# Kernel optimization log

Hardware: AMD Instinct MI355X
Metric: run time of the kernel (lower is better)

## Reference

```python
import jax, jax.numpy as jnp
import numpy as np
from jax import lax

# mamba-130m-style config
B, L = 2, 1024          # batch, seq_len
D = 768                 # hidden_size
E = 1536                # intermediate (expand=2)
N = 16                  # ssm state size
R = 48                  # time_step_rank = ceil(D/16)
K = 4                   # conv kernel
NL = 4                  # num layers
NC = 5                  # num classes
EPS = 1e-5


def setup_inputs() -> dict:
    key = jax.random.key(0)
    ks = jax.random.split(key, 10)
    s = 0.02
    return {
        "x": jax.random.normal(ks[0], (B, L, 12), dtype=jnp.float32),
        "proj_w": jax.random.normal(ks[1], (D, 12)) * s,
        "proj_b": jnp.zeros((D,), jnp.float32),
        "norm_w": jnp.ones((NL, D), jnp.float32),
        "in_w": jax.random.normal(ks[2], (NL, 2 * E, D)) * s,
        "conv_w": jax.random.normal(ks[3], (NL, E, K)) * s,
        "conv_b": jnp.zeros((NL, E), jnp.float32),
        "xproj_w": jax.random.normal(ks[4], (NL, R + 2 * N, E)) * s,
        "dt_w": jax.random.normal(ks[5], (NL, E, R)) * s,
        "dt_b": jnp.full((NL, E), -4.0, jnp.float32),  # softplus(-4) ~ small dt
        "A_log": jnp.tile(jnp.log(jnp.arange(1, N + 1, dtype=jnp.float32))[None, None, :], (NL, E, 1)),
        "D_param": jnp.ones((NL, E), jnp.float32),
        "out_w": jax.random.normal(ks[6], (NL, D, E)) * s,
        "fnorm_w": jnp.ones((D,), jnp.float32),
        "cls_w": jax.random.normal(ks[7], (NC, D)) * s,
        "cls_b": jnp.zeros((NC,), jnp.float32),
    }


def _rmsnorm(x, w):
    var = jnp.mean(x * x, axis=-1, keepdims=True)
    return x * lax.rsqrt(var + EPS) * w


def _causal_conv(u, w, b):
    # u: [B,L,E], w: [E,K] depthwise causal conv, left-pad K-1
    up = jnp.pad(u, ((0, 0), (K - 1, 0), (0, 0)))
    y = b
    for k in range(K):
        y = y + w[:, k] * up[:, k:k + L, :]
    return y


def _selective_scan(u, dt, A, Bm, Cm, Dp):
    # u, dt: [B,L,E]; Bm, Cm: [B,L,N]; A: [E,N]; Dp: [E]
    def step(h, inp):
        u_t, dt_t, B_t, C_t = inp  # [B,E],[B,E],[B,N],[B,N]
        dA = jnp.exp(dt_t[:, :, None] * A)                      # [B,E,N]
        h = h * dA + dt_t[:, :, None] * B_t[:, None, :] * u_t[:, :, None]
        y = jnp.einsum('ben,bn->be', h, C_t)
        return h, y

    h0 = jnp.zeros((u.shape[0], E, N), u.dtype)
    _, ys = lax.scan(step, h0,
                     (u.transpose(1, 0, 2), dt.transpose(1, 0, 2),
                      Bm.transpose(1, 0, 2), Cm.transpose(1, 0, 2)))
    return ys.transpose(1, 0, 2) + u * Dp


def reference(x, proj_w, proj_b, norm_w, in_w, conv_w, conv_b, xproj_w,
              dt_w, dt_b, A_log, D_param, out_w, fnorm_w, cls_w, cls_b):
    h = x @ proj_w.T + proj_b                                     # [B,L,D]
    for i in range(NL):
        res = h
        hn = _rmsnorm(h, norm_w[i])
        proj = hn @ in_w[i].T                                     # [B,L,2E]
        u, gate = proj[..., :E], proj[..., E:]
        u = jax.nn.silu(_causal_conv(u, conv_w[i], conv_b[i]))    # [B,L,E]
        xdbc = u @ xproj_w[i].T                                   # [B,L,R+2N]
        dt_r = xdbc[..., :R]
        Bm = xdbc[..., R:R + N]
        Cm = xdbc[..., R + N:]
        dt = jax.nn.softplus(dt_r @ dt_w[i].T + dt_b[i])          # [B,L,E]
        A = -jnp.exp(A_log[i])                                    # [E,N]
        y = _selective_scan(u, dt, A, Bm, Cm, D_param[i])
        y = y * jax.nn.silu(gate)
        h = res + y @ out_w[i].T
    h = _rmsnorm(h, fnorm_w)
    pooled = jnp.mean(h, axis=1)                                  # AdaptiveAvgPool1d(1)
    return pooled @ cls_w.T + cls_b                               # [B,NC]
```

## Files before the change

kernel.cpp:

```cpp
#include <hip/hip_runtime.h>

constexpr int B_  = 2;
constexpr int L_  = 1024;
constexpr int D_  = 768;
constexpr int E_  = 1536;
constexpr int N_  = 16;
constexpr int R_  = 48;
constexpr int NL_ = 4;
constexpr int NC_ = 5;
constexpr int M_  = B_ * L_;
constexpr int E2_ = 2 * E_;
constexpr int XD_ = R_ + 2 * N_;
constexpr float EPS_ = 1e-5f;

constexpr int NCH_ = 16;
constexpr int CL_  = L_ / NCH_;
constexpr int KS_  = 8;
constexpr int PC_  = 8;

typedef __attribute__((ext_vector_type(8))) short bf16x8;
typedef __attribute__((ext_vector_type(4))) float f32x4;
typedef const __attribute__((address_space(1))) void* gas_t;
typedef __attribute__((address_space(3))) void* las_t;

__device__ __forceinline__ float sigm(float x) { return 1.0f / (1.0f + __expf(-x)); }
__device__ __forceinline__ float softplusf(float x) { return x > 20.0f ? x : log1pf(__expf(x)); }
__device__ __forceinline__ ushort f2b(float f) {
  union { float f; unsigned u; } v; v.f = f;
  unsigned r = (v.u + 0x7fffu + ((v.u >> 16) & 1u)) >> 16;
  return (ushort)r;
}
__device__ __forceinline__ float b2f(ushort u) {
  union { unsigned u; float f; } v; v.u = ((unsigned)u) << 16;
  return v.f;
}
__device__ __forceinline__ float b2f_lo(unsigned p) {
  union { unsigned u; float f; } v; v.u = p << 16;
  return v.f;
}
__device__ __forceinline__ float b2f_hi(unsigned p) {
  union { unsigned u; float f; } v; v.u = p & 0xffff0000u;
  return v.f;
}

template <int CTRL>
__device__ __forceinline__ float dpp_add(float x) {
  int yi = __builtin_amdgcn_update_dpp(0, __builtin_bit_cast(int, x), CTRL, 0xf, 0xf, false);
  return x + __builtin_bit_cast(float, yi);
}
__device__ __forceinline__ float row_sum16(float x) {
  x = dpp_add<0x121>(x);
  x = dpp_add<0x122>(x);
  x = dpp_add<0x124>(x);
  x = dpp_add<0x128>(x);
  return x;
}

__device__ __forceinline__ float block_sum(float v, float* sm) {
  #pragma unroll
  for (int o = 32; o > 0; o >>= 1) v += __shfl_xor(v, o);
  if ((threadIdx.x & 63) == 0) sm[threadIdx.x >> 6] = v;
  __syncthreads();
  return sm[0] + sm[1] + sm[2] + sm[3];
}

constexpr int WS1_ = NL_ * E2_ * D_;
constexpr int WS2_ = NL_ * D_ * E_;
constexpr int WS3_ = NL_ * XD_ * E_;
constexpr int WS4_ = NL_ * E_ * 64;
constexpr int WTOT_ = WS1_ + WS2_ + WS3_ + WS4_;
constexpr int WB_ = WTOT_ / 4 / 256;
__global__ __launch_bounds__(256) void k_wprep(const float* __restrict__ in_w, const float* __restrict__ out_w,
                                               const float* __restrict__ xw, const float* __restrict__ dw,
                                               ushort* __restrict__ in_wb, ushort* __restrict__ out_wb,
                                               ushort* __restrict__ xwb, ushort* __restrict__ dtwb,
                                               const float* __restrict__ x, const float* __restrict__ pw,
                                               const float* __restrict__ pb, float* __restrict__ h) {
  if (blockIdx.x >= WB_) {
    __shared__ float xs[12];
    int bx = blockIdx.x - WB_;
    int m = bx / 3;
    int d = (bx % 3) * 256 + threadIdx.x;
    if (threadIdx.x < 12) xs[threadIdx.x] = x[m * 12 + threadIdx.x];
    __syncthreads();
    float acc = pb[d];
    #pragma unroll
    for (int j = 0; j < 12; j++) acc = fmaf(xs[j], pw[d * 12 + j], acc);
    h[(size_t)m * D_ + d] = acc;
    return;
  }
  int i = (blockIdx.x * 256 + threadIdx.x) * 4;
  if (i < WS1_) {
    float4 v = *(const float4*)(in_w + i);
    *(ushort4*)(in_wb + i) = make_ushort4(f2b(v.x), f2b(v.y), f2b(v.z), f2b(v.w));
  } else if (i < WS1_ + WS2_) {
    int j = i - WS1_;
    float4 v = *(const float4*)(out_w + j);
    *(ushort4*)(out_wb + j) = make_ushort4(f2b(v.x), f2b(v.y), f2b(v.z), f2b(v.w));
  } else if (i < WS1_ + WS2_ + WS3_) {
    int j = i - WS1_ - WS2_;
    float4 v = *(const float4*)(xw + j);
    *(ushort4*)(xwb + j) = make_ushort4(f2b(v.x), f2b(v.y), f2b(v.z), f2b(v.w));
  } else {
    int j = i - WS1_ - WS2_ - WS3_;
    int k = j & 63, e = j >> 6;
    ushort4 o;
    o.x = (k + 0 < R_) ? f2b(dw[e * R_ + k + 0]) : (ushort)0;
    o.y = (k + 1 < R_) ? f2b(dw[e * R_ + k + 1]) : (ushort)0;
    o.z = (k + 2 < R_) ? f2b(dw[e * R_ + k + 2]) : (ushort)0;
    o.w = (k + 3 < R_) ? f2b(dw[e * R_ + k + 3]) : (ushort)0;
    *(ushort4*)(dtwb + j) = o;
  }
}

__global__ __launch_bounds__(256) void k_rmsnorm_bf(const float* __restrict__ h, const float* __restrict__ w,
                                                    ushort* __restrict__ hn) {
  __shared__ float sm[4];
  int m = blockIdx.x, tid = threadIdx.x;
  const float* row = h + (size_t)m * D_;
  float v0 = row[tid], v1 = row[tid + 256], v2 = row[tid + 512];
  float s = block_sum(v0 * v0 + v1 * v1 + v2 * v2, sm);
  float sc = rsqrtf(s * (1.0f / D_) + EPS_);
  ushort* o = hn + (size_t)m * D_;
  o[tid]       = f2b(v0 * sc * w[tid]);
  o[tid + 256] = f2b(v1 * sc * w[tid + 256]);
  o[tid + 512] = f2b(v2 * sc * w[tid + 512]);
}

template <int BM, int BN, int MODE>
__global__ __launch_bounds__(256) void k_gemm_bf(const ushort* __restrict__ A, const ushort* __restrict__ Bw,
                                                 void* __restrict__ Cv, const float* __restrict__ res,
                                                 int Kd, int Nd) {
  constexpr int AM = BM / 32, BNF = BN / 32;
  __shared__ ushort sA[BM * 32];
  __shared__ ushort sB[BN * 32];
  const int tid = threadIdx.x;
  const int wave = tid >> 6, lane = tid & 63;
  const int q = lane >> 4, r = lane & 15;
  const int wm = wave >> 1, wn = wave & 1;
  const int m0 = blockIdx.y * BM, n0 = blockIdx.x * BN;
  f32x4 acc[AM][BNF] = {};

  for (int k0 = 0; k0 < Kd; k0 += 32) {
    #pragma unroll
    for (int j = 0; j < BM / 64; j++) {
      int i = j * 256 + tid;
      const ushort* gp = A + (size_t)(m0 + (i >> 2)) * Kd + k0 + ((i & 3) << 3);
      __builtin_amdgcn_global_load_lds((gas_t)gp, (las_t)(sA + ((j * 256 + wave * 64) << 3)), 16, 0, 0);
    }
    #pragma unroll
    for (int j = 0; j < BN / 64; j++) {
      int i = j * 256 + tid;
      const ushort* gp = Bw + (size_t)(n0 + (i >> 2)) * Kd + k0 + ((i & 3) << 3);
      __builtin_amdgcn_global_load_lds((gas_t)gp, (las_t)(sB + ((j * 256 + wave * 64) << 3)), 16, 0, 0);
    }
    __syncthreads();
    bf16x8 af[AM], bfv[BNF];
    #pragma unroll
    for (int mi = 0; mi < AM; mi++)
      af[mi] = *(const bf16x8*)&sA[(wm * (BM / 2) + mi * 16 + r) * 32 + q * 8];
    #pragma unroll
    for (int nj = 0; nj < BNF; nj++)
      bfv[nj] = *(const bf16x8*)&sB[(wn * (BN / 2) + nj * 16 + r) * 32 + q * 8];
    #pragma unroll
    for (int mi = 0; mi < AM; mi++)
      #pragma unroll
      for (int nj = 0; nj < BNF; nj++)
        acc[mi][nj] = __builtin_amdgcn_mfma_f32_16x16x32_bf16(af[mi], bfv[nj], acc[mi][nj], 0, 0, 0);
    __syncthreads();
  }
  #pragma unroll
  for (int mi = 0; mi < AM; mi++) {
    #pragma unroll
    for (int nj = 0; nj < BNF; nj++) {
      int col = n0 + wn * (BN / 2) + nj * 16 + r;
      #pragma unroll
      for (int rg = 0; rg < 4; rg++) {
        int row = m0 + wm * (BM / 2) + mi * 16 + q * 4 + rg;
        size_t off = (size_t)row * Nd + col;
        float v = acc[mi][nj][rg];
        if (MODE == 3) {
          ((ushort*)Cv)[off] = f2b(v);
        } else {
          if (MODE == 1) v += res[off];
          if (MODE == 2) v = softplusf(v + res[col]);
          ((float*)Cv)[off] = v;
        }
      }
    }
  }
}

__global__ __launch_bounds__(256) void k_gemm_x(const ushort* __restrict__ A, const ushort* __restrict__ Bw,
                                                float* __restrict__ part) {
  __shared__ ushort sA[64 * 32];
  __shared__ ushort sB[80 * 32];
  const int tid = threadIdx.x;
  const int wave = tid >> 6, lane = tid & 63;
  const int q = lane >> 4, r = lane & 15;
  const int m0 = blockIdx.x * 64;
  const int kbeg = blockIdx.y * (E_ / KS_), kend = kbeg + E_ / KS_;
  f32x4 acc[5] = {};

  for (int k0 = kbeg; k0 < kend; k0 += 32) {
    {
      const ushort* gp = A + (size_t)(m0 + wave * 16 + (lane >> 2)) * E_ + k0 + ((lane & 3) << 3);
      __builtin_amdgcn_global_load_lds((gas_t)gp, (las_t)(sA + (wave << 9)), 16, 0, 0);
    }
    #pragma unroll
    for (int j = wave; j < 5; j += 4) {
      const ushort* gp = Bw + (size_t)(j * 16 + (lane >> 2)) * E_ + k0 + ((lane & 3) << 3);
      __builtin_amdgcn_global_load_lds((gas_t)gp, (las_t)(sB + (j << 9)), 16, 0, 0);
    }
    __syncthreads();
    bf16x8 af = *(const bf16x8*)&sA[(wave * 16 + r) * 32 + q * 8];
    #pragma unroll
    for (int nj = 0; nj < 5; nj++) {
      bf16x8 bfv = *(const bf16x8*)&sB[(nj * 16 + r) * 32 + q * 8];
      acc[nj] = __builtin_amdgcn_mfma_f32_16x16x32_bf16(af, bfv, acc[nj], 0, 0, 0);
    }
    __syncthreads();
  }
  float* pp = part + (size_t)blockIdx.y * M_ * XD_;
  #pragma unroll
  for (int nj = 0; nj < 5; nj++) {
    int col = nj * 16 + r;
    #pragma unroll
    for (int rg = 0; rg < 4; rg++) {
      int row = m0 + wave * 16 + q * 4 + rg;
      pp[(size_t)row * XD_ + col] = acc[nj][rg];
    }
  }
}

__global__ __launch_bounds__(256) void k_xfin(const float* __restrict__ part, float* __restrict__ xdbc,
                                              ushort* __restrict__ xb) {
  int i = blockIdx.x * 256 + threadIdx.x;
  int m = i / XD_, col = i - m * XD_;
  float s = 0.0f;
  #pragma unroll
  for (int ks = 0; ks < KS_; ks++) s += part[(size_t)ks * M_ * XD_ + i];
  xdbc[i] = s;
  if (col < R_) xb[(size_t)m * 64 + col] = f2b(s);
  else if (col < 64) xb[(size_t)m * 64 + col] = 0;
}

__global__ __launch_bounds__(384) void k_conv2(const ushort* __restrict__ proj, const float* __restrict__ cw,
                                               const float* __restrict__ cb, ushort* __restrict__ ub16,
                                               ushort* __restrict__ gb16) {
  int m = blockIdx.x;
  int b = m >> 10, t = m & (L_ - 1);
  int e4 = threadIdx.x * 4;
  float wv[4][4];
  #pragma unroll
  for (int j = 0; j < 4; j++) {
    float4 w = *(const float4*)(cw + (e4 + j) * 4);
    wv[j][0] = w.x; wv[j][1] = w.y; wv[j][2] = w.z; wv[j][3] = w.w;
  }
  float4 bb = *(const float4*)(cb + e4);
  float acc[4] = {bb.x, bb.y, bb.z, bb.w};
  #pragma unroll
  for (int k = 0; k < 4; k++) {
    int tt = t + k - 3;
    if (tt >= 0) {
      uint2 p = *(const uint2*)(proj + (size_t)(b * L_ + tt) * E2_ + e4);
      acc[0] = fmaf(wv[0][k], b2f_lo(p.x), acc[0]);
      acc[1] = fmaf(wv[1][k], b2f_hi(p.x), acc[1]);
      acc[2] = fmaf(wv[2][k], b2f_lo(p.y), acc[2]);
      acc[3] = fmaf(wv[3][k], b2f_hi(p.y), acc[3]);
    }
  }
  uint2 uo;
  {
    float u0 = acc[0] * sigm(acc[0]), u1 = acc[1] * sigm(acc[1]);
    float u2 = acc[2] * sigm(acc[2]), u3 = acc[3] * sigm(acc[3]);
    uo.x = (unsigned)f2b(u0) | ((unsigned)f2b(u1) << 16);
    uo.y = (unsigned)f2b(u2) | ((unsigned)f2b(u3) << 16);
  }
  *(uint2*)(ub16 + (size_t)m * E_ + e4) = uo;
  uint2 g = *(const uint2*)(proj + (size_t)m * E2_ + E_ + e4);
  float g0 = b2f_lo(g.x), g1 = b2f_hi(g.x), g2 = b2f_lo(g.y), g3 = b2f_hi(g.y);
  g0 *= sigm(g0); g1 *= sigm(g1); g2 *= sigm(g2); g3 *= sigm(g3);
  uint2 go;
  go.x = (unsigned)f2b(g0) | ((unsigned)f2b(g1) << 16);
  go.y = (unsigned)f2b(g2) | ((unsigned)f2b(g3) << 16);
  *(uint2*)(gb16 + (size_t)m * E_ + e4) = go;
}

__global__ __launch_bounds__(256, 6) void k_scanA(const ushort* __restrict__ u, const float* __restrict__ dtb,
                                                  const float* __restrict__ xdbc, const float* __restrict__ A_log,
                                                  float* __restrict__ Pst, float* __restrict__ Sst) {
  __shared__ float2 s_dtu[CL_][16];
  __shared__ float  s_b [CL_][16];
  const int tid = threadIdx.x;
  const int e0 = blockIdx.x << 4;
  const int b  = blockIdx.y;
  const int c  = blockIdx.z;
  const int n  = tid & 15, el = tid >> 4;
  const int e  = e0 + el;
  const float A = -__expf(A_log[e * N_ + n]);
  const int t0 = c * CL_;

  float r_dt[4], r_b[4];
  ushort r_u[4];
  #pragma unroll
  for (int j = 0; j < 4; j++) {
    size_t m = (size_t)(b * L_ + t0 + j * 16 + el);
    r_dt[j] = dtb[m * E_ + e0 + n];
    r_u[j]  = u[m * E_ + e0 + n];
    int idx = j * 256 + tid;
    r_b[j] = xdbc[(size_t)(b * L_ + t0 + (idx >> 4)) * XD_ + R_ + (idx & 15)];
  }
  #pragma unroll
  for (int j = 0; j < 4; j++) {
    int t = j * 16 + el;
    s_dtu[t][n] = make_float2(r_dt[j], r_dt[j] * b2f(r_u[j]));
    int idx = j * 256 + tid;
    s_b[idx >> 4][idx & 15] = r_b[j];
  }
  __syncthreads();

  float hs = 0.0f, pp = 1.0f;
  #pragma unroll 8
  for (int t = 0; t < CL_; t++) {
    float2 dtu = s_dtu[t][el];
    float dA = __expf(dtu.x * A);
    hs = fmaf(hs, dA, dtu.y * s_b[t][n]);
    pp *= dA;
  }
  size_t o = (((size_t)(b * NCH_ + c) * E_) + e) * N_ + n;
  Pst[o] = pp;
  Sst[o] = hs;
}

__global__ __launch_bounds__(256, 6) void k_scanC(const ushort* __restrict__ u, const float* __restrict__ dtb,
                                                  const float* __restrict__ xdbc, const ushort* __restrict__ gb,
                                                  const float* __restrict__ A_log, const float* __restrict__ Dp,
                                                  const float* __restrict__ Pst, const float* __restrict__ Sst,
                                                  ushort* __restrict__ y) {
  __shared__ float2 s_dtu[CL_][16];
  __shared__ float2 s_bc [CL_][16];
  __shared__ float2 s_og [CL_][16];
  __shared__ ushort s_y [CL_][16];
  const int tid = threadIdx.x;
  const int e0 = blockIdx.x << 4;
  const int b  = blockIdx.y;
  const int c  = blockIdx.z;
  const int n  = tid & 15, el = tid >> 4;
  const int e  = e0 + el;
  const float A = -__expf(A_log[e * N_ + n]);
  const float Dv = Dp[e0 + n];
  const int t0 = c * CL_;

  float r_dt[4], r_bc[8];
  ushort r_u[4], r_g[4];
  #pragma unroll
  for (int j = 0; j < 4; j++) {
    size_t m = (size_t)(b * L_ + t0 + j * 16 + el);
    r_dt[j] = dtb[m * E_ + e0 + n];
    r_u[j]  = u[m * E_ + e0 + n];
    r_g[j]  = gb[m * E_ + e0 + n];
  }
  #pragma unroll
  for (int j = 0; j < 8; j++) {
    int idx = j * 256 + tid;
    r_bc[j] = xdbc[(size_t)(b * L_ + t0 + (idx >> 5)) * XD_ + R_ + (idx & 31)];
  }

  float hs = 0.0f;
  if (c > 0) {
    float pv[NCH_ - 1], sv[NCH_ - 1];
    #pragma unroll
    for (int cc = 0; cc < NCH_ - 1; cc++) {
      int ci = cc < c ? cc : c - 1;
      size_t o = (((size_t)(b * NCH_ + ci) * E_) + e) * N_ + n;
      pv[cc] = Pst[o];
      sv[cc] = Sst[o];
    }
    #pragma unroll
    for (int cc = 0; cc < NCH_ - 1; cc++) {
      bool v = cc < c;
      hs = fmaf(v ? pv[cc] : 1.0f, hs, v ? sv[cc] : 0.0f);
    }
  }

  #pragma unroll
  for (int j = 0; j < 4; j++) {
    int t = j * 16 + el;
    float uf = b2f(r_u[j]);
    s_dtu[t][n] = make_float2(r_dt[j], r_dt[j] * uf);
    s_og[t][n] = make_float2(uf * Dv, b2f(r_g[j]));
  }
  #pragma unroll
  for (int j = 0; j < 8; j++) {
    int idx = j * 256 + tid;
    int t = idx >> 5, col = idx & 31;
    ((float*)&s_bc[t][0])[((col & 15) << 1) + (col >> 4)] = r_bc[j];
  }
  __syncthreads();

  #pragma unroll 8
  for (int t = 0; t < CL_; t++) {
    float2 dtu = s_dtu[t][el];
    float2 bc  = s_bc[t][n];
    float dA = __expf(dtu.x * A);
    hs = fmaf(hs, dA, dtu.y * bc.x);
    float p = row_sum16(hs * bc.y);
    if (n == 0) {
      float2 og = s_og[t][el];
      s_y[t][el] = f2b((p + og.x) * og.y);
    }
  }
  __syncthreads();

  {
    int row = tid >> 2, seg = tid & 3;
    uint2 v = *(const uint2*)&s_y[row][seg * 4];
    *(uint2*)(y + (size_t)(b * L_ + t0 + row) * E_ + e0 + seg * 4) = v;
  }
}

__global__ __launch_bounds__(256) void k_rowscale(const float* __restrict__ h, float* __restrict__ rs) {
  __shared__ float sm[4];
  int m = blockIdx.x, tid = threadIdx.x;
  const float* row = h + (size_t)m * D_;
  float v0 = row[tid], v1 = row[tid + 256], v2 = row[tid + 512];
  float s = block_sum(v0 * v0 + v1 * v1 + v2 * v2, sm);
  if (tid == 0) rs[m] = rsqrtf(s * (1.0f / D_) + EPS_);
}

__global__ __launch_bounds__(256) void k_pool(const float* __restrict__ h, const float* __restrict__ rs,
                                              float* __restrict__ pooledP) {
  int d = blockIdx.x * 256 + threadIdx.x;
  int pc = blockIdx.y;
  int b = blockIdx.z;
  int t0 = pc * (L_ / PC_);
  float acc = 0.0f;
  for (int t = t0; t < t0 + L_ / PC_; t++) {
    int m = b * L_ + t;
    acc = fmaf(h[(size_t)m * D_ + d], rs[m], acc);
  }
  pooledP[((size_t)pc * B_ + b) * D_ + d] = acc;
}

__global__ __launch_bounds__(256) void k_logits(const float* __restrict__ pooledP, const float* __restrict__ fw,
                                                const float* __restrict__ cw, const float* __restrict__ cb,
                                                float* __restrict__ out) {
  __shared__ float sp[B_ * D_];
  int tid = threadIdx.x;
  for (int d = tid; d < B_ * D_; d += 256) {
    int b = d / D_, dd = d - b * D_;
    float pd = 0.0f;
    #pragma unroll
    for (int pc = 0; pc < PC_; pc++) pd += pooledP[((size_t)pc * B_ + b) * D_ + dd];
    sp[d] = pd * fw[dd] * (1.0f / L_);
  }
  __syncthreads();
  int wv = tid >> 6, ln = tid & 63;
  for (int p = wv; p < B_ * NC_; p += 4) {
    int b = p / NC_, c = p % NC_;
    float s = 0.0f;
    for (int d = ln; d < D_; d += 64) s = fmaf(sp[b * D_ + d], cw[c * D_ + d], s);
    #pragma unroll
    for (int o = 32; o > 0; o >>= 1) s += __shfl_xor(s, o);
    if (ln == 0) out[p] = s + cb[c];
  }
}

extern "C" void kernel_launch(void* const* d_in, const int* in_sizes, int n_in,
                              void* d_out, int out_size, void* d_ws, size_t ws_size,
                              hipStream_t stream) {
  const float* x       = (const float*)d_in[0];
  const float* proj_w  = (const float*)d_in[1];
  const float* proj_b  = (const float*)d_in[2];
  const float* norm_w  = (const float*)d_in[3];
  const float* in_w    = (const float*)d_in[4];
  const float* conv_w  = (const float*)d_in[5];
  const float* conv_b  = (const float*)d_in[6];
  const float* xproj_w = (const float*)d_in[7];
  const float* dt_w    = (const float*)d_in[8];
  const float* dt_b    = (const float*)d_in[9];
  const float* A_log   = (const float*)d_in[10];
  const float* D_param = (const float*)d_in[11];
  const float* out_w   = (const float*)d_in[12];
  const float* fnorm_w = (const float*)d_in[13];
  const float* cls_w   = (const float*)d_in[14];
  const float* cls_b   = (const float*)d_in[15];
  float* out = (float*)d_out;

  float* h      = (float*)d_ws;
  float* xdbc   = h + (size_t)M_ * D_;
  float* dtbuf  = xdbc + (size_t)M_ * XD_;
  float* rsb    = dtbuf + (size_t)M_ * E_;
  float* pooledP = rsb + M_;
  float* Pst    = pooledP + (size_t)PC_ * B_ * D_;
  float* Sst    = Pst + (size_t)B_ * NCH_ * E_ * N_;
  float* xpart  = Sst + (size_t)B_ * NCH_ * E_ * N_;
  ushort* proj_bf = (ushort*)(xpart + (size_t)KS_ * M_ * XD_);
  ushort* hn_bf   = proj_bf + (size_t)M_ * E2_;
  ushort* y_bf    = hn_bf + (size_t)M_ * D_;
  ushort* ub_bf   = y_bf + (size_t)M_ * E_;
  ushort* g_bf    = ub_bf + (size_t)M_ * E_;
  ushort* xdbc_bf = g_bf + (size_t)M_ * E_;
  ushort* xwb     = xdbc_bf + (size_t)M_ * 64;
  ushort* dtwb    = xwb + (size_t)NL_ * XD_ * E_;
  ushort* in_wb   = dtwb + (size_t)NL_ * E_ * 64;
  ushort* out_wb  = in_wb + (size_t)NL_ * E2_ * D_;

  k_wprep<<<WB_ + 3 * M_, 256, 0, stream>>>(in_w, out_w, xproj_w, dt_w,
                                            in_wb, out_wb, xwb, dtwb,
                                            x, proj_w, proj_b, h);

  for (int i = 0; i < NL_; i++) {
    k_rmsnorm_bf<<<M_, 256, 0, stream>>>(h, norm_w + i * D_, hn_bf);
    k_gemm_bf<64, 192, 3><<<dim3(E2_ / 192, M_ / 64), 256, 0, stream>>>(
        hn_bf, in_wb + (size_t)i * E2_ * D_, proj_bf, nullptr, D_, E2_);
    k_conv2<<<M_, 384, 0, stream>>>(proj_bf, conv_w + i * E_ * 4, conv_b + i * E_, ub_bf, g_bf);
    k_gemm_x<<<dim3(M_ / 64, KS_), 256, 0, stream>>>(ub_bf, xwb + (size_t)i * XD_ * E_, xpart);
    k_xfin<<<M_ * XD_ / 256, 256, 0, stream>>>(xpart, xdbc, xdbc_bf);
    k_gemm_bf<64, 64, 2><<<dim3(E_ / 64, M_ / 64), 256, 0, stream>>>(
        xdbc_bf, dtwb + (size_t)i * E_ * 64, dtbuf, dt_b + i * E_, 64, E_);
    k_scanA<<<dim3(E_ / 16, B_, NCH_), 256, 0, stream>>>(ub_bf, dtbuf, xdbc,
                                                         A_log + (size_t)i * E_ * N_, Pst, Sst);
    k_scanC<<<dim3(E_ / 16, B_, NCH_), 256, 0, stream>>>(ub_bf, dtbuf, xdbc, g_bf,
                                                         A_log + (size_t)i * E_ * N_, D_param + i * E_,
                                                         Pst, Sst, y_bf);
    k_gemm_bf<64, 64, 1><<<dim3(D_ / 64, M_ / 64), 256, 0, stream>>>(
        y_bf, out_wb + (size_t)i * D_ * E_, h, h, E_, D_);
  }

  k_rowscale<<<M_, 256, 0, stream>>>(h, rsb);
  k_pool<<<dim3(D_ / 256, PC_, B_), 256, 0, stream>>>(h, rsb, pooledP);
  k_logits<<<1, 256, 0, stream>>>(pooledP, fnorm_w, cls_w, cls_b, out);
}
```

Baseline: 675.5 us.

## Fold RMSNorm into in-proj GEMM and fuse sum-of-squares into out-proj epilogue

Drops the per-layer RMSNorm kernel. The norm weight is folded into the bf16 in_proj weights at prep time, and the per-row rsqrt scale is applied in the in_proj GEMM epilogue (MODE 4). The out_proj GEMM epilogue now writes h in both fp32 and bf16 and atomically accumulates each row's sum of squares for the next layer; k_xfin zeroes that buffer. The change also retiles the in_proj GEMM to 128x128 and makes the conv kernel handle 4 timesteps per block so neighbouring inputs are reused. The cost is atomics, and the input to the GEMM is now unnormalised h in bf16, which changes rounding.

Result: no change. 669.8 us (-0.9%).

```diff
diff --git a/kernel.cpp b/kernel.cpp
--- a/kernel.cpp
+++ b/kernel.cpp
@@ -72,10 +72,12 @@
 constexpr int WB_ = WTOT_ / 4 / 256;
 __global__ __launch_bounds__(256) void k_wprep(const float* __restrict__ in_w, const float* __restrict__ out_w,
                                                const float* __restrict__ xw, const float* __restrict__ dw,
+                                               const float* __restrict__ nw,
                                                ushort* __restrict__ in_wb, ushort* __restrict__ out_wb,
                                                ushort* __restrict__ xwb, ushort* __restrict__ dtwb,
                                                const float* __restrict__ x, const float* __restrict__ pw,
-                                               const float* __restrict__ pb, float* __restrict__ h) {
+                                               const float* __restrict__ pb, float* __restrict__ h,
+                                               ushort* __restrict__ hb) {
   if (blockIdx.x >= WB_) {
     __shared__ float xs[12];
     int bx = blockIdx.x - WB_;
@@ -87,12 +89,16 @@
     #pragma unroll
     for (int j = 0; j < 12; j++) acc = fmaf(xs[j], pw[d * 12 + j], acc);
     h[(size_t)m * D_ + d] = acc;
+    hb[(size_t)m * D_ + d] = f2b(acc);
     return;
   }
   int i = (blockIdx.x * 256 + threadIdx.x) * 4;
   if (i < WS1_) {
     float4 v = *(const float4*)(in_w + i);
-    *(ushort4*)(in_wb + i) = make_ushort4(f2b(v.x), f2b(v.y), f2b(v.z), f2b(v.w));
+    int l = i / (E2_ * D_);
+    int d = i % D_;
+    float4 w = *(const float4*)(nw + l * D_ + d);
+    *(ushort4*)(in_wb + i) = make_ushort4(f2b(v.x * w.x), f2b(v.y * w.y), f2b(v.z * w.z), f2b(v.w * w.w));
   } else if (i < WS1_ + WS2_) {
     int j = i - WS1_;
     float4 v = *(const float4*)(out_w + j);
@@ -113,23 +119,19 @@
   }
 }
 
-__global__ __launch_bounds__(256) void k_rmsnorm_bf(const float* __restrict__ h, const float* __restrict__ w,
-                                                    ushort* __restrict__ hn) {
+__global__ __launch_bounds__(256) void k_sumsq(const float* __restrict__ h, float* __restrict__ ssq) {
   __shared__ float sm[4];
   int m = blockIdx.x, tid = threadIdx.x;
   const float* row = h + (size_t)m * D_;
   float v0 = row[tid], v1 = row[tid + 256], v2 = row[tid + 512];
   float s = block_sum(v0 * v0 + v1 * v1 + v2 * v2, sm);
-  float sc = rsqrtf(s * (1.0f / D_) + EPS_);
-  ushort* o = hn + (size_t)m * D_;
-  o[tid]       = f2b(v0 * sc * w[tid]);
-  o[tid + 256] = f2b(v1 * sc * w[tid + 256]);
-  o[tid + 512] = f2b(v2 * sc * w[tid + 512]);
+  if (tid == 0) ssq[m] = s;
 }
 
 template <int BM, int BN, int MODE>
 __global__ __launch_bounds__(256) void k_gemm_bf(const ushort* __restrict__ A, const ushort* __restrict__ Bw,
                                                  void* __restrict__ Cv, const float* __restrict__ res,
+                                                 ushort* __restrict__ Cb, float* __restrict__ ssq,
                                                  int Kd, int Nd) {
   constexpr int AM = BM / 32, BNF = BN / 32;
   __shared__ ushort sA[BM * 32];
@@ -172,20 +174,33 @@
   #pragma unroll
   for (int mi = 0; mi < AM; mi++) {
     #pragma unroll
-    for (int nj = 0; nj < BNF; nj++) {
-      int col = n0 + wn * (BN / 2) + nj * 16 + r;
+    for (int rg = 0; rg < 4; rg++) {
+      int row = m0 + wm * (BM / 2) + mi * 16 + q * 4 + rg;
+      float rs = 0.0f, ssl = 0.0f;
+      if (MODE == 4) rs = rsqrtf(res[row] * (1.0f / D_) + EPS_);
       #pragma unroll
-      for (int rg = 0; rg < 4; rg++) {
-        int row = m0 + wm * (BM / 2) + mi * 16 + q * 4 + rg;
+      for (int nj = 0; nj < BNF; nj++) {
+        int col = n0 + wn * (BN / 2) + nj * 16 + r;
         size_t off = (size_t)row * Nd + col;
         float v = acc[mi][nj][rg];
         if (MODE == 3) {
           ((ushort*)Cv)[off] = f2b(v);
+        } else if (MODE == 4) {
+          ((ushort*)Cv)[off] = f2b(v * rs);
+        } else if (MODE == 5) {
+          v += res[off];
+          ((float*)Cv)[off] = v;
+          Cb[off] = f2b(v);
+          ssl = fmaf(v, v, ssl);
         } else {
           if (MODE == 1) v += res[off];
           if (MODE == 2) v = softplusf(v + res[col]);
           ((float*)Cv)[off] = v;
         }
+      }
+      if (MODE == 5) {
+        float sr = row_sum16(ssl);
+        if (r == 0) atomicAdd(&ssq[row], sr);
       }
     }
   }
@@ -234,8 +249,9 @@
 }
 
 __global__ __launch_bounds__(256) void k_xfin(const float* __restrict__ part, float* __restrict__ xdbc,
-                                              ushort* __restrict__ xb) {
+                                              ushort* __restrict__ xb, float* __restrict__ ssq) {
   int i = blockIdx.x * 256 + threadIdx.x;
+  if (i < M_) ssq[i] = 0.0f;
   int m = i / XD_, col = i - m * XD_;
   float s = 0.0f;
   #pragma unroll
@@ -245,11 +261,13 @@
   else if (col < 64) xb[(size_t)m * 64 + col] = 0;
 }
 
+constexpr int TC_ = 4;
 __global__ __launch_bounds__(384) void k_conv2(const ushort* __restrict__ proj, const float* __restrict__ cw,
                                                const float* __restrict__ cb, ushort* __restrict__ ub16,
                                                ushort* __restrict__ gb16) {
-  int m = blockIdx.x;
-  int b = m >> 10, t = m & (L_ - 1);
+  int m0 = blockIdx.x * TC_;
+  int t0 = m0 & (L_ - 1);
+  int base = m0 - t0;
   int e4 = threadIdx.x * 4;
   float wv[4][4];
   #pragma unroll
@@ -258,33 +276,56 @@
     wv[j][0] = w.x; wv[j][1] = w.y; wv[j][2] = w.z; wv[j][3] = w.w;
   }
   float4 bb = *(const float4*)(cb + e4);
-  float acc[4] = {bb.x, bb.y, bb.z, bb.w};
-  #pragma unroll
-  for (int k = 0; k < 4; k++) {
-    int tt = t + k - 3;
-    if (tt >= 0) {
-      uint2 p = *(const uint2*)(proj + (size_t)(b * L_ + tt) * E2_ + e4);
-      acc[0] = fmaf(wv[0][k], b2f_lo(p.x), acc[0]);
-      acc[1] = fmaf(wv[1][k], b2f_hi(p.x), acc[1]);
-      acc[2] = fmaf(wv[2][k], b2f_lo(p.y), acc[2]);
-      acc[3] = fmaf(wv[3][k], b2f_hi(p.y), acc[3]);
-    }
-  }
-  uint2 uo;
-  {
-    float u0 = acc[0] * sigm(acc[0]), u1 = acc[1] * sigm(acc[1]);
-    float u2 = acc[2] * sigm(acc[2]), u3 = acc[3] * sigm(acc[3]);
-    uo.x = (unsigned)f2b(u0) | ((unsigned)f2b(u1) << 16);
-    uo.y = (unsigned)f2b(u2) | ((unsigned)f2b(u3) << 16);
-  }
-  *(uint2*)(ub16 + (size_t)m * E_ + e4) = uo;
-  uint2 g = *(const uint2*)(proj + (size_t)m * E2_ + E_ + e4);
-  float g0 = b2f_lo(g.x), g1 = b2f_hi(g.x), g2 = b2f_lo(g.y), g3 = b2f_hi(g.y);
-  g0 *= sigm(g0); g1 *= sigm(g1); g2 *= sigm(g2); g3 *= sigm(g3);
-  uint2 go;
-  go.x = (unsigned)f2b(g0) | ((unsigned)f2b(g1) << 16);
-  go.y = (unsigned)f2b(g2) | ((unsigned)f2b(g3) << 16);
-  *(uint2*)(gb16 + (size_t)m * E_ + e4) = go;
+  float bbv[4] = {bb.x, bb.y, bb.z, bb.w};
+  float win[4][4];
+  #pragma unroll
+  for (int s = 0; s < 3; s++) {
+    int t = t0 - 3 + s;
+    if (t >= 0) {
+      uint2 p = *(const uint2*)(proj + (size_t)(base + t) * E2_ + e4);
+      win[s][0] = b2f_lo(p.x); win[s][1] = b2f_hi(p.x);
+      win[s][2] = b2f_lo(p.y); win[s][3] = b2f_hi(p.y);
+    } else {
+      win[s][0] = win[s][1] = win[s][2] = win[s][3] = 0.0f;
+    }
+  }
+  #pragma unroll
+  for (int j = 0; j < TC_; j++) {
+    size_t m = (size_t)(m0 + j);
+    uint2 p = *(const uint2*)(proj + m * E2_ + e4);
+    win[3][0] = b2f_lo(p.x); win[3][1] = b2f_hi(p.x);
+    win[3][2] = b2f_lo(p.y); win[3][3] = b2f_hi(p.y);
+    float o[4];
+    #pragma unroll
+    for (int c = 0; c < 4; c++) {
+      float a = bbv[c];
+      a = fmaf(wv[c][0], win[0][c], a);
+      a = fmaf(wv[c][1], win[1][c], a);
+      a = fmaf(wv[c][2], win[2][c], a);
+      a = fmaf(wv[c][3], win[3][c], a);
+      o[c] = a * sigm(a);
+    }
+    uint2 uo;
+    uo.x = (unsigned)f2b(o[0]) | ((unsigned)f2b(o[1]) << 16);
+    uo.y = (unsigned)f2b(o[2]) | ((unsigned)f2b(o[3]) << 16);
+    *(uint2*)(ub16 + m * E_ + e4) = uo;
+    #pragma unroll
+    for (int s = 0; s < 3; s++) {
+      win[s][0] = win[s + 1][0]; win[s][1] = win[s + 1][1];
+      win[s][2] = win[s + 1][2]; win[s][3] = win[s + 1][3];
+    }
+  }
+  #pragma unroll
+  for (int j = 0; j < TC_; j++) {
+    size_t m = (size_t)(m0 + j);
+    uint2 g = *(const uint2*)(proj + m * E2_ + E_ + e4);
+    float g0 = b2f_lo(g.x), g1 = b2f_hi(g.x), g2 = b2f_lo(g.y), g3 = b2f_hi(g.y);
+    g0 *= sigm(g0); g1 *= sigm(g1); g2 *= sigm(g2); g3 *= sigm(g3);
+    uint2 go;
+    go.x = (unsigned)f2b(g0) | ((unsigned)f2b(g1) << 16);
+    go.y = (unsigned)f2b(g2) | ((unsigned)f2b(g3) << 16);
+    *(uint2*)(gb16 + m * E_ + e4) = go;
+  }
 }
 
 __global__ __launch_bounds__(256, 6) void k_scanA(const ushort* __restrict__ u, const float* __restrict__ dtb,
@@ -492,13 +533,14 @@
   float* xdbc   = h + (size_t)M_ * D_;
   float* dtbuf  = xdbc + (size_t)M_ * XD_;
   float* rsb    = dtbuf + (size_t)M_ * E_;
-  float* pooledP = rsb + M_;
+  float* ssq    = rsb + M_;
+  float* pooledP = ssq + M_;
   float* Pst    = pooledP + (size_t)PC_ * B_ * D_;
   float* Sst    = Pst + (size_t)B_ * NCH_ * E_ * N_;
   float* xpart  = Sst + (size_t)B_ * NCH_ * E_ * N_;
   ushort* proj_bf = (ushort*)(xpart + (size_t)KS_ * M_ * XD_);
-  ushort* hn_bf   = proj_bf + (size_t)M_ * E2_;
-  ushort* y_bf    = hn_bf + (size_t)M_ * D_;
+  ushort* hb_bf   = proj_bf + (size_t)M_ * E2_;
+  ushort* y_bf    = hb_bf + (size_t)M_ * D_;
   ushort* ub_bf   = y_bf + (size_t)M_ * E_;
   ushort* g_bf    = ub_bf + (size_t)M_ * E_;
   ushort* xdbc_bf = g_bf + (size_t)M_ * E_;
@@ -507,26 +549,26 @@
   ushort* in_wb   = dtwb + (size_t)NL_ * E_ * 64;
   ushort* out_wb  = in_wb + (size_t)NL_ * E2_ * D_;
 
-  k_wprep<<<WB_ + 3 * M_, 256, 0, stream>>>(in_w, out_w, xproj_w, dt_w,
+  k_wprep<<<WB_ + 3 * M_, 256, 0, stream>>>(in_w, out_w, xproj_w, dt_w, norm_w,
                                             in_wb, out_wb, xwb, dtwb,
-                                            x, proj_w, proj_b, h);
+                                            x, proj_w, proj_b, h, hb_bf);
+  k_sumsq<<<M_, 256, 0, stream>>>(h, ssq);
 
   for (int i = 0; i < NL_; i++) {
-    k_rmsnorm_bf<<<M_, 256, 0, stream>>>(h, norm_w + i * D_, hn_bf);
-    k_gemm_bf<64, 192, 3><<<dim3(E2_ / 192, M_ / 64), 256, 0, stream>>>(
-        hn_bf, in_wb + (size_t)i * E2_ * D_, proj_bf, nullptr, D_, E2_);
-    k_conv2<<<M_, 384, 0, stream>>>(proj_bf, conv_w + i * E_ * 4, conv_b + i * E_, ub_bf, g_bf);
+    k_gemm_bf<128, 128, 4><<<dim3(E2_ / 128, M_ / 128), 256, 0, stream>>>(
+        hb_bf, in_wb + (size_t)i * E2_ * D_, proj_bf, ssq, nullptr, nullptr, D_, E2_);
+    k_conv2<<<M_ / TC_, 384, 0, stream>>>(proj_bf, conv_w + i * E_ * 4, conv_b + i * E_, ub_bf, g_bf);
     k_gemm_x<<<dim3(M_ / 64, KS_), 256, 0, stream>>>(ub_bf, xwb + (size_t)i * XD_ * E_, xpart);
-    k_xfin<<<M_ * XD_ / 256, 256, 0, stream>>>(xpart, xdbc, xdbc_bf);
+    k_xfin<<<M_ * XD_ / 256, 256, 0, stream>>>(xpart, xdbc, xdbc_bf, ssq);
     k_gemm_bf<64, 64, 2><<<dim3(E_ / 64, M_ / 64), 256, 0, stream>>>(
-        xdbc_bf, dtwb + (size_t)i * E_ * 64, dtbuf, dt_b + i * E_, 64, E_);
+        xdbc_bf, dtwb + (size_t)i * E_ * 64, dtbuf, dt_b + i * E_, nullptr, nullptr, 64, E_);
     k_scanA<<<dim3(E_ / 16, B_, NCH_), 256, 0, stream>>>(ub_bf, dtbuf, xdbc,
                                                          A_log + (size_t)i * E_ * N_, Pst, Sst);
     k_scanC<<<dim3(E_ / 16, B_, NCH_), 256, 0, stream>>>(ub_bf, dtbuf, xdbc, g_bf,
                                                          A_log + (size_t)i * E_ * N_, D_param + i * E_,
                                                          Pst, Sst, y_bf);
-    k_gemm_bf<64, 64, 1><<<dim3(D_ / 64, M_ / 64), 256, 0, stream>>>(
-        y_bf, out_wb + (size_t)i * D_ * E_, h, h, E_, D_);
+    k_gemm_bf<64, 64, 5><<<dim3(D_ / 64, M_ / 64), 256, 0, stream>>>(
+        y_bf, out_wb + (size_t)i * D_ * E_, h, h, hb_bf, ssq, E_, D_);
   }
 
   k_rowscale<<<M_, 256, 0, stream>>>(h, rsb);
```
